# Performance work log

Hardware: AMD Instinct MI355X
Metric: run time of the kernel (lower is better)

The kernel has to match this reference:

```python
import jax, jax.numpy as jnp
import numpy as np

D_MODEL = 1024
HEADS = 16


def setup_inputs() -> dict:
    key = jax.random.key(0)
    ks = jax.random.split(key, 5)
    S = 4096
    x = jax.random.normal(ks[0], (S, D_MODEL), dtype=jnp.float32)
    scale = 1.0 / np.sqrt(D_MODEL)
    Wq = jax.random.normal(ks[1], (D_MODEL, D_MODEL), dtype=jnp.float32) * scale
    Wk = jax.random.normal(ks[2], (D_MODEL, D_MODEL), dtype=jnp.float32) * scale
    Wv = jax.random.normal(ks[3], (D_MODEL, D_MODEL), dtype=jnp.float32) * scale
    Wo = jax.random.normal(ks[4], (D_MODEL, D_MODEL), dtype=jnp.float32) * scale
    return {"x": x, "Wq": Wq, "Wk": Wk, "Wv": Wv, "Wo": Wo}


def reference(x, Wq, Wk, Wv, Wo):
    # x: [S, D]; weights follow torch Linear convention y = x @ W.T
    S, D = x.shape
    H = HEADS
    d_k = D // H
    q = (x @ Wq.T).reshape(S, H, d_k)  # [S,H,dk]
    k = (x @ Wk.T).reshape(S, H, d_k)
    v = (x @ Wv.T).reshape(S, H, d_k)
    # logits: [H, S, S] = q k^T / sqrt(d_k)
    logits = jnp.einsum('shd,thd->hst', q, k) / jnp.sqrt(jnp.asarray(d_k, x.dtype))
    probs = jax.nn.softmax(logits, axis=-1)
    out = jnp.einsum('hst,thd->shd', probs, v).reshape(S, D)
    return out @ Wo.T
```

## Files before the change

kernel.cpp:

```cpp
#include <hip/hip_runtime.h>
#include <hip/hip_bf16.h>


typedef __bf16 bf16_t;
typedef __bf16 bf16x8 __attribute__((ext_vector_type(8)));
typedef __bf16 bf16x4 __attribute__((ext_vector_type(4)));
typedef float f32x4 __attribute__((ext_vector_type(4)));

#define D_MODEL 1024
#define SEQ 4096
#define HEADS 16
#define DK 64
#define QSCALE 0.1803368801111204f
#define EXP2_MAGIC 8404859.0f

__global__ void cast_kernel(const float* __restrict__ in, bf16_t* __restrict__ out, int n) {
    int i = (blockIdx.x * blockDim.x + threadIdx.x) * 4;
    if (i < n) {
        float4 v = *(const float4*)(in + i);
        bf16x4 o;
        o[0] = (bf16_t)v.x; o[1] = (bf16_t)v.y; o[2] = (bf16_t)v.z; o[3] = (bf16_t)v.w;
        *(bf16x4*)(out + i) = o;
    }
}

__global__ void cast4_kernel(const float* __restrict__ a, const float* __restrict__ b,
                             const float* __restrict__ c, const float* __restrict__ d,
                             bf16_t* __restrict__ out) {
    int gi = blockIdx.x * blockDim.x + threadIdx.x;
    int which = gi >> 18;
    int i = (gi & 0x3FFFF) * 4;
    const float* src = which == 0 ? a : which == 1 ? b : which == 2 ? c : d;
    float4 v = *(const float4*)(src + i);
    bf16x4 o;
    o[0] = (bf16_t)v.x; o[1] = (bf16_t)v.y; o[2] = (bf16_t)v.z; o[3] = (bf16_t)v.w;
    *(bf16x4*)(out + (size_t)which * D_MODEL * D_MODEL + i) = o;
}

__device__ __forceinline__ void g2l16(const bf16_t* g, bf16_t* l) {
    __builtin_amdgcn_global_load_lds(
        (const __attribute__((address_space(1))) void*)g,
        (__attribute__((address_space(3))) void*)l, 16, 0, 0);
}

__device__ __forceinline__ bf16x8 exp2_pk(const f32x4 a, const f32x4 b) {
    union { float f; unsigned u; } v[8];
#pragma unroll
    for (int r = 0; r < 4; r++) {
        v[r].f     = fmaf(a[r], 128.0f, EXP2_MAGIC);
        v[r + 4].f = fmaf(b[r], 128.0f, EXP2_MAGIC);
    }
    union { unsigned u[4]; bf16x8 h; } o;
#pragma unroll
    for (int p = 0; p < 4; p++)
        o.u[p] = __builtin_amdgcn_perm(v[2 * p + 1].u, v[2 * p].u, 0x05040100u);
    return o.h;
}

template <int ROUTE>
__global__ __launch_bounds__(256, 2) void gemm_lds(const bf16_t* __restrict__ A,
                                                   const bf16_t* __restrict__ B,
                                                   void* __restrict__ out0,
                                                   void* __restrict__ out1,
                                                   void* __restrict__ out2,
                                                   int M, int N, int K) {
    __shared__ __align__(16) bf16_t As[128 * 64];
    __shared__ __align__(16) bf16_t Bs[128 * 64];

    const int tid = threadIdx.x;
    const int lane = tid & 63;
    const int wave = tid >> 6;
    const int l15 = lane & 15;
    const int lg  = lane >> 4;
    const int m0 = blockIdx.y * 128;
    const int n0 = blockIdx.x * 128;
    const int wm = (wave >> 1) * 64;
    const int wn = (wave & 1) * 64;

    const bf16_t* aSrc[4]; bf16_t* aDst[4];
    const bf16_t* bSrc[4]; bf16_t* bDst[4];
#pragma unroll
    for (int it = 0; it < 4; it++) {
        int c = it * 256 + tid;
        int row = c >> 3, cc = (c & 7) ^ (row & 7);
        aSrc[it] = A + (size_t)(m0 + row) * K + cc * 8;
        aDst[it] = As + c * 8;
        bSrc[it] = B + (size_t)(n0 + row) * K + cc * 8;
        bDst[it] = Bs + c * 8;
    }

    int aoff[2][4], boff[2][4];
#pragma unroll
    for (int kk = 0; kk < 2; kk++) {
#pragma unroll
        for (int i = 0; i < 4; i++) {
            int row = wm + i * 16 + l15;
            aoff[kk][i] = row * 64 + (((kk << 2) | lg) ^ (row & 7)) * 8;
        }
#pragma unroll
        for (int j = 0; j < 4; j++) {
            int row = wn + j * 16 + l15;
            boff[kk][j] = row * 64 + (((kk << 2) | lg) ^ (row & 7)) * 8;
        }
    }

    f32x4 acc[4][4];
#pragma unroll
    for (int i = 0; i < 4; i++)
#pragma unroll
        for (int j = 0; j < 4; j++) acc[i][j] = f32x4{0.f, 0.f, 0.f, 0.f};

    for (int k0 = 0; k0 < K; k0 += 64) {
#pragma unroll
        for (int it = 0; it < 4; it++) g2l16(aSrc[it] + k0, aDst[it]);
#pragma unroll
        for (int it = 0; it < 4; it++) g2l16(bSrc[it] + k0, bDst[it]);
        __syncthreads();

#pragma unroll
        for (int kk = 0; kk < 2; kk++) {
            bf16x8 af[4], bfm[4];
#pragma unroll
            for (int i = 0; i < 4; i++) af[i] = *(const bf16x8*)(As + aoff[kk][i]);
#pragma unroll
            for (int j = 0; j < 4; j++) bfm[j] = *(const bf16x8*)(Bs + boff[kk][j]);
#pragma unroll
            for (int i = 0; i < 4; i++)
#pragma unroll
                for (int j = 0; j < 4; j++)
                    acc[i][j] = __builtin_amdgcn_mfma_f32_16x16x32_bf16(af[i], bfm[j], acc[i][j], 0, 0, 0);
        }
        __syncthreads();
    }

    const int ng = n0 + wn;
    if (ROUTE == 0) {
        float* C = (float*)out0;
#pragma unroll
        for (int i = 0; i < 4; i++)
#pragma unroll
            for (int r = 0; r < 4; r++) {
                int m = m0 + wm + i * 16 + lg * 4 + r;
                float* crow = C + (size_t)m * N + ng;
#pragma unroll
                for (int j = 0; j < 4; j++) crow[j * 16 + l15] = acc[i][j][r];
            }
    } else {
        if (ng < 2048) {
            const bool isQ = (ng < 1024);
            const float sc = isQ ? QSCALE : 1.0f;
            bf16_t* dst = isQ ? (bf16_t*)out0 : (bf16_t*)out1;
            int nn = ng & 1023;
#pragma unroll
            for (int i = 0; i < 4; i++)
#pragma unroll
                for (int r = 0; r < 4; r++) {
                    int m = m0 + wm + i * 16 + lg * 4 + r;
                    bf16_t* crow = dst + (size_t)m * D_MODEL + nn;
#pragma unroll
                    for (int j = 0; j < 4; j++) crow[j * 16 + l15] = (bf16_t)(acc[i][j][r] * sc);
                }
        } else {
            bf16_t* Vt = (bf16_t*)out2;
#pragma unroll
            for (int i = 0; i < 4; i++)
#pragma unroll
                for (int j = 0; j < 4; j++) {
                    int vcol = ng - 2048 + j * 16 + l15;
                    int m = m0 + wm + i * 16 + lg * 4;
                    int mp = (m & ~31) | (((m >> 2) & 3) << 3) | (((m >> 4) & 1) << 2);
                    bf16x4 v4;
#pragma unroll
                    for (int r = 0; r < 4; r++) v4[r] = (bf16_t)acc[i][j][r];
                    *(bf16x4*)(Vt + (size_t)vcol * SEQ + mp) = v4;
                }
        }
    }
}

__global__ __launch_bounds__(512, 2) void attn_kernel(const bf16_t* __restrict__ Q,
                                                      const bf16_t* __restrict__ Km,
                                                      const bf16_t* __restrict__ Vt,
                                                      bf16_t* __restrict__ O) {
    const int tid = threadIdx.x;
    const int lane = tid & 63;
    const int wave = tid >> 6;
    const int l15 = lane & 15;
    const int lg  = lane >> 4;
    const int bid = blockIdx.x;
    const int h    = (bid & 7) * 2 + ((bid >> 3) & 1);
    const int qblk = bid >> 4;
    const int q0 = qblk * 256;
    const int hoff = h * DK;

    __shared__ struct {
        __align__(16) bf16_t K[3][64 * 64];
        __align__(16) bf16_t V[3][64 * 64];
    } sm;

    bf16x8 qf[2][2];
#pragma unroll
    for (int t = 0; t < 2; t++)
#pragma unroll
        for (int c = 0; c < 2; c++)
            qf[t][c] = *(const bf16x8*)(Q + (size_t)(q0 + wave * 32 + t * 16 + l15) * D_MODEL
                                        + hoff + c * 32 + lg * 8);

    f32x4 oacc[2][4], lfrag[2];
#pragma unroll
    for (int t = 0; t < 2; t++) {
        lfrag[t] = f32x4{0.f, 0.f, 0.f, 0.f};
#pragma unroll
        for (int dt = 0; dt < 4; dt++) oacc[t][dt] = f32x4{0.f, 0.f, 0.f, 0.f};
    }

    bf16x8 ones8;
#pragma unroll
    for (int j = 0; j < 8; j++) ones8[j] = (bf16_t)1.0f;

    const int srow = tid >> 3;
    const int sdc = (tid & 7) ^ (srow & 7);
    const bf16_t* kSrc = Km + (size_t)srow * D_MODEL + hoff + sdc * 8;
    const bf16_t* vSrc = Vt + (size_t)(hoff + srow) * SEQ + sdc * 8;

    int kOff[4][2], vOff[2][4];
#pragma unroll
    for (int kt = 0; kt < 4; kt++)
#pragma unroll
        for (int c = 0; c < 2; c++) {
            int row = kt * 16 + l15;
            kOff[kt][c] = row * 64 + (((c * 4 + lg) ^ (row & 7)) * 8);
        }
#pragma unroll
    for (int kp = 0; kp < 2; kp++)
#pragma unroll
        for (int dt = 0; dt < 4; dt++) {
            int row = dt * 16 + l15;
            vOff[kp][dt] = row * 64 + (((kp * 4 + lg) ^ (row & 7)) * 8);
        }

    g2l16(kSrc,                           &sm.K[0][tid * 8]);
    g2l16(vSrc,                           &sm.V[0][tid * 8]);
    g2l16(kSrc + (size_t)64 * D_MODEL,    &sm.K[1][tid * 8]);
    g2l16(vSrc + 64,                      &sm.V[1][tid * 8]);

    int cur = 0, nb = 2;
    for (int s = 0; s < SEQ / 64; s++) {
        asm volatile("s_waitcnt vmcnt(2)" ::: "memory");
        __builtin_amdgcn_s_barrier();

        const int s2 = (s + 2) & (SEQ / 64 - 1);
        g2l16(kSrc + (size_t)s2 * 64 * D_MODEL, &sm.K[nb][tid * 8]);
        g2l16(vSrc + s2 * 64,                   &sm.V[nb][tid * 8]);

        const bf16_t* Kb = sm.K[cur];
        const bf16_t* Vb = sm.V[cur];

        __builtin_amdgcn_s_setprio(1);
#pragma unroll
        for (int kp = 0; kp < 2; kp++) {
            bf16x8 vf[4];
#pragma unroll
            for (int dt = 0; dt < 4; dt++) vf[dt] = *(const bf16x8*)(Vb + vOff[kp][dt]);

            f32x4 st[2][2];
#pragma unroll
            for (int sub = 0; sub < 2; sub++) {
                const int kt = kp * 2 + sub;
                const bf16x8 kf0 = *(const bf16x8*)(Kb + kOff[kt][0]);
                const bf16x8 kf1 = *(const bf16x8*)(Kb + kOff[kt][1]);
#pragma unroll
                for (int t = 0; t < 2; t++) {
                    f32x4 a = f32x4{0.f, 0.f, 0.f, 0.f};
                    a = __builtin_amdgcn_mfma_f32_16x16x32_bf16(kf0, qf[t][0], a, 0, 0, 0);
                    a = __builtin_amdgcn_mfma_f32_16x16x32_bf16(kf1, qf[t][1], a, 0, 0, 0);
                    st[t][sub] = a;
                }
            }

#pragma unroll
            for (int t = 0; t < 2; t++) {
                const bf16x8 pbig = exp2_pk(st[t][0], st[t][1]);
                lfrag[t] = __builtin_amdgcn_mfma_f32_16x16x32_bf16(ones8, pbig, lfrag[t], 0, 0, 0);
#pragma unroll
                for (int dt = 0; dt < 4; dt++)
                    oacc[t][dt] = __builtin_amdgcn_mfma_f32_16x16x32_bf16(vf[dt], pbig, oacc[t][dt], 0, 0, 0);
            }
        }
        __builtin_amdgcn_s_setprio(0);

        cur = (cur == 2) ? 0 : cur + 1;
        nb  = (nb  == 2) ? 0 : nb + 1;
    }

#pragma unroll
    for (int t = 0; t < 2; t++) {
        const float inv = 1.f / lfrag[t][0];
        const size_t qrow = (size_t)(q0 + wave * 32 + t * 16 + l15);
#pragma unroll
        for (int dt = 0; dt < 4; dt++) {
            bf16x4 o4;
#pragma unroll
            for (int r = 0; r < 4; r++) o4[r] = (bf16_t)(oacc[t][dt][r] * inv);
            *(bf16x4*)(O + qrow * D_MODEL + hoff + dt * 16 + lg * 4) = o4;
        }
    }
}

extern "C" void kernel_launch(void* const* d_in, const int* in_sizes, int n_in,
                              void* d_out, int out_size, void* d_ws, size_t ws_size,
                              hipStream_t stream) {
    const float* x  = (const float*)d_in[0];
    const float* Wq = (const float*)d_in[1];
    const float* Wk = (const float*)d_in[2];
    const float* Wv = (const float*)d_in[3];
    const float* Wo = (const float*)d_in[4];
    float* out = (float*)d_out;

    char* ws = (char*)d_ws;
    bf16_t* xb  = (bf16_t*)(ws);
    bf16_t* wqb = (bf16_t*)(ws + (8u  << 20));
    bf16_t* wob = (bf16_t*)(ws + (14u << 20));
    bf16_t* Qb  = (bf16_t*)(ws + (16u << 20));
    bf16_t* Kb  = (bf16_t*)(ws + (24u << 20));
    bf16_t* Vtb = (bf16_t*)(ws + (32u << 20));
    bf16_t* Ab  = (bf16_t*)(ws + (40u << 20));

    const int nX = SEQ * D_MODEL;
    cast_kernel<<<nX / 4 / 256, 256, 0, stream>>>(x, xb, nX);
    cast4_kernel<<<4 * 1024, 256, 0, stream>>>(Wq, Wk, Wv, Wo, wqb);

    gemm_lds<1><<<dim3(3 * D_MODEL / 128, SEQ / 128), 256, 0, stream>>>(
        xb, wqb, Qb, Kb, Vtb, SEQ, 3 * D_MODEL, D_MODEL);

    attn_kernel<<<256, 512, 0, stream>>>(Qb, Kb, Vtb, Ab);

    gemm_lds<0><<<dim3(D_MODEL / 128, SEQ / 128), 256, 0, stream>>>(
        Ab, wob, out, nullptr, nullptr, SEQ, D_MODEL, D_MODEL);
}
```

Before: 191.6 us.

## Merge cast kernels, XCD-aware GEMM tile mapping, double-buffer attention K/V loads

Folds the x cast and the four weight casts into a single launch. Remaps GEMM block indices so each XCD handles a contiguous band of M rows, aiming for better L2 reuse. Cuts the attention kernel from a 3-stage to a 2-stage LDS pipeline with __syncthreads and drops the s_setprio hints, which shortens the prefetch distance and may expose more load latency.

New measurement: 185.4 us. 1.03x faster.

```diff
diff --git a/kernel.cpp b/kernel.cpp
--- a/kernel.cpp
+++ b/kernel.cpp
@@ -14,27 +14,25 @@
 #define QSCALE 0.1803368801111204f
 #define EXP2_MAGIC 8404859.0f
 
-__global__ void cast_kernel(const float* __restrict__ in, bf16_t* __restrict__ out, int n) {
-    int i = (blockIdx.x * blockDim.x + threadIdx.x) * 4;
-    if (i < n) {
-        float4 v = *(const float4*)(in + i);
-        bf16x4 o;
-        o[0] = (bf16_t)v.x; o[1] = (bf16_t)v.y; o[2] = (bf16_t)v.z; o[3] = (bf16_t)v.w;
-        *(bf16x4*)(out + i) = o;
-    }
-}
-
-__global__ void cast4_kernel(const float* __restrict__ a, const float* __restrict__ b,
-                             const float* __restrict__ c, const float* __restrict__ d,
-                             bf16_t* __restrict__ out) {
-    int gi = blockIdx.x * blockDim.x + threadIdx.x;
-    int which = gi >> 18;
-    int i = (gi & 0x3FFFF) * 4;
-    const float* src = which == 0 ? a : which == 1 ? b : which == 2 ? c : d;
+__global__ void cast_all(const float* __restrict__ x, const float* __restrict__ a,
+                         const float* __restrict__ b, const float* __restrict__ c,
+                         const float* __restrict__ d, bf16_t* __restrict__ xb,
+                         bf16_t* __restrict__ wb) {
+    const int gi = blockIdx.x * blockDim.x + threadIdx.x;
+    const float* src; bf16_t* dst; int i;
+    if (gi < SEQ * D_MODEL / 4) {
+        src = x; dst = xb; i = gi * 4;
+    } else {
+        int g = gi - SEQ * D_MODEL / 4;
+        int which = g >> 18;
+        src = which == 0 ? a : which == 1 ? b : which == 2 ? c : d;
+        dst = wb + (size_t)which * D_MODEL * D_MODEL;
+        i = (g & 0x3FFFF) * 4;
+    }
     float4 v = *(const float4*)(src + i);
     bf16x4 o;
     o[0] = (bf16_t)v.x; o[1] = (bf16_t)v.y; o[2] = (bf16_t)v.z; o[3] = (bf16_t)v.w;
-    *(bf16x4*)(out + (size_t)which * D_MODEL * D_MODEL + i) = o;
+    *(bf16x4*)(dst + i) = o;
 }
 
 __device__ __forceinline__ void g2l16(const bf16_t* g, bf16_t* l) {
@@ -72,8 +70,13 @@
     const int wave = tid >> 6;
     const int l15 = lane & 15;
     const int lg  = lane >> 4;
-    const int m0 = blockIdx.y * 128;
-    const int n0 = blockIdx.x * 128;
+
+    const int flat = blockIdx.y * gridDim.x + blockIdx.x;
+    const int mpx  = gridDim.y >> 3;
+    const int xcd  = flat & 7;
+    const int pos  = flat >> 3;
+    const int m0 = (xcd * mpx + (pos % mpx)) * 128;
+    const int n0 = (pos / mpx) * 128;
     const int wm = (wave >> 1) * 64;
     const int wn = (wave & 1) * 64;
 
@@ -194,8 +197,8 @@
     const int hoff = h * DK;
 
     __shared__ struct {
-        __align__(16) bf16_t K[3][64 * 64];
-        __align__(16) bf16_t V[3][64 * 64];
+        __align__(16) bf16_t K[2][64 * 64];
+        __align__(16) bf16_t V[2][64 * 64];
     } sm;
 
     bf16x8 qf[2][2];
@@ -239,24 +242,22 @@
             vOff[kp][dt] = row * 64 + (((kp * 4 + lg) ^ (row & 7)) * 8);
         }
 
-    g2l16(kSrc,                           &sm.K[0][tid * 8]);
-    g2l16(vSrc,                           &sm.V[0][tid * 8]);
-    g2l16(kSrc + (size_t)64 * D_MODEL,    &sm.K[1][tid * 8]);
-    g2l16(vSrc + 64,                      &sm.V[1][tid * 8]);
-
-    int cur = 0, nb = 2;
+    g2l16(kSrc, &sm.K[0][tid * 8]);
+    g2l16(vSrc, &sm.V[0][tid * 8]);
+
     for (int s = 0; s < SEQ / 64; s++) {
-        asm volatile("s_waitcnt vmcnt(2)" ::: "memory");
-        __builtin_amdgcn_s_barrier();
-
-        const int s2 = (s + 2) & (SEQ / 64 - 1);
-        g2l16(kSrc + (size_t)s2 * 64 * D_MODEL, &sm.K[nb][tid * 8]);
-        g2l16(vSrc + s2 * 64,                   &sm.V[nb][tid * 8]);
+        const int cur = s & 1;
+        __syncthreads();
+
+        if (s + 1 < SEQ / 64) {
+            const int nxt = cur ^ 1;
+            g2l16(kSrc + (size_t)(s + 1) * 64 * D_MODEL, &sm.K[nxt][tid * 8]);
+            g2l16(vSrc + (s + 1) * 64,                   &sm.V[nxt][tid * 8]);
+        }
 
         const bf16_t* Kb = sm.K[cur];
         const bf16_t* Vb = sm.V[cur];
 
-        __builtin_amdgcn_s_setprio(1);
 #pragma unroll
         for (int kp = 0; kp < 2; kp++) {
             bf16x8 vf[4];
@@ -287,10 +288,6 @@
                     oacc[t][dt] = __builtin_amdgcn_mfma_f32_16x16x32_bf16(vf[dt], pbig, oacc[t][dt], 0, 0, 0);
             }
         }
-        __builtin_amdgcn_s_setprio(0);
-
-        cur = (cur == 2) ? 0 : cur + 1;
-        nb  = (nb  == 2) ? 0 : nb + 1;
     }
 
 #pragma unroll
@@ -326,9 +323,7 @@
     bf16_t* Vtb = (bf16_t*)(ws + (32u << 20));
     bf16_t* Ab  = (bf16_t*)(ws + (40u << 20));
 
-    const int nX = SEQ * D_MODEL;
-    cast_kernel<<<nX / 4 / 256, 256, 0, stream>>>(x, xb, nX);
-    cast4_kernel<<<4 * 1024, 256, 0, stream>>>(Wq, Wk, Wv, Wo, wqb);
+    cast_all<<<8192, 256, 0, stream>>>(x, Wq, Wk, Wv, Wo, xb, wqb);
 
     gemm_lds<1><<<dim3(3 * D_MODEL / 128, SEQ / 128), 256, 0, stream>>>(
         xb, wqb, Qb, Kb, Vtb, SEQ, 3 * D_MODEL, D_MODEL);
```
